# Kernel tuning notes

Hardware: AMD Instinct MI355X
Metric: run time of the kernel (lower is better)

Reference implementation:

```python
import jax, jax.numpy as jnp
import numpy as np

HIDDEN = 1024
SCALE = float(np.sqrt(HIDDEN))  # canonical sqrt(d) scale factor


def setup_inputs() -> dict:
    key = jax.random.key(0)
    ks = jax.random.split(key, 10)
    B, S, D = 4, 2048, HIDDEN
    bound = 1.0 / np.sqrt(D)  # torch Linear default init range
    inp = {
        "q": jax.random.normal(ks[0], (B, S, D), dtype=jnp.float32),
        "k": jax.random.normal(ks[1], (B, S, D), dtype=jnp.float32),
        "v": jax.random.normal(ks[2], (B, S, D), dtype=jnp.float32),
        "mask": jnp.zeros((B, S, S), dtype=bool),  # unused by original forward
        "Wq": jax.random.uniform(ks[3], (D, D), jnp.float32, -bound, bound),
        "bq": jax.random.uniform(ks[4], (D,), jnp.float32, -bound, bound),
        "Wk": jax.random.uniform(ks[5], (D, D), jnp.float32, -bound, bound),
        "bk": jax.random.uniform(ks[6], (D,), jnp.float32, -bound, bound),
        "Wv": jax.random.uniform(ks[7], (D, D), jnp.float32, -bound, bound),
        "bv": jax.random.uniform(ks[8], (D,), jnp.float32, -bound, bound),
    }
    return inp


def reference(q, k, v, mask, Wq, bq, Wk, bk, Wv, bv):
    # torch Linear: y = x @ W.T + b
    qp = jnp.einsum("bsd,ed->bse", q, Wq) + bq  # [B,S,D]
    kp = jnp.einsum("bsd,ed->bse", k, Wk) + bk
    vp = jnp.einsum("bsd,ed->bse", v, Wv) + bv
    scores = jnp.einsum("bqd,bkd->bqk", qp, kp) / SCALE  # [B,S,S]
    attn = jax.nn.softmax(scores, axis=-1)
    # dropout with p=0 (dropout_p undefined in source) -> identity
    out = jnp.einsum("bqk,bkd->bqd", attn, vp)  # [B,S,D]
    return out
```

## Files before the change

kernel.cpp:

```cpp
#include <hip/hip_runtime.h>

#define S_ 2048
#define D_ 1024
#define MTOT 8192

typedef __attribute__((ext_vector_type(8))) short bf16x8;
typedef __attribute__((ext_vector_type(8))) unsigned short ush8;
typedef __attribute__((ext_vector_type(4))) unsigned short ush4;
typedef __attribute__((ext_vector_type(4))) float f32x4;

__device__ __forceinline__ unsigned short f2bf(float x) {
    unsigned u = __builtin_bit_cast(unsigned, x);
    u += 0x7fffu + ((u >> 16) & 1u);
    return (unsigned short)(u >> 16);
}

__device__ __forceinline__ void async16(const unsigned short* g, unsigned short* l) {
    __builtin_amdgcn_global_load_lds(
        (const __attribute__((address_space(1))) unsigned int*)(g),
        (__attribute__((address_space(3))) unsigned int*)(l),
        16, 0, 0);
}

#define FENCE() asm volatile("" ::: "memory")
#define SBAR()  __builtin_amdgcn_s_barrier()
#define SCHED0() __builtin_amdgcn_sched_barrier(0)

template<int N> __device__ __forceinline__ void waitv();
template<> __device__ __forceinline__ void waitv<0>() { asm volatile("s_waitcnt vmcnt(0)" ::: "memory"); }
template<> __device__ __forceinline__ void waitv<2>() { asm volatile("s_waitcnt vmcnt(2)" ::: "memory"); }
template<> __device__ __forceinline__ void waitv<4>() { asm volatile("s_waitcnt vmcnt(4)" ::: "memory"); }

__device__ __forceinline__ int xcd_remap(int id, int nwg) {
    return (id & 7) * (nwg >> 3) + (id >> 3);
}

__global__ __launch_bounds__(256)
void tobf16_kernel(const float* __restrict__ s0, const float* __restrict__ s1,
                   const float* __restrict__ s2, const float* __restrict__ s3,
                   const float* __restrict__ s4, const float* __restrict__ s5,
                   unsigned short* __restrict__ d0, unsigned short* __restrict__ d1,
                   unsigned short* __restrict__ d2, unsigned short* __restrict__ d3,
                   unsigned short* __restrict__ d4, unsigned short* __restrict__ d5)
{
    const float* src; unsigned short* dst; size_t n;
    switch (blockIdx.y) {
        case 0: src = s0; dst = d0; n = (size_t)MTOT * D_; break;
        case 1: src = s1; dst = d1; n = (size_t)MTOT * D_; break;
        case 2: src = s2; dst = d2; n = (size_t)MTOT * D_; break;
        case 3: src = s3; dst = d3; n = (size_t)D_ * D_;   break;
        case 4: src = s4; dst = d4; n = (size_t)D_ * D_;   break;
        default: src = s5; dst = d5; n = (size_t)D_ * D_;  break;
    }
    size_t base = ((size_t)blockIdx.x * 256 + threadIdx.x) * 8;
    if (base >= n) return;
    float4 a = *reinterpret_cast<const float4*>(src + base);
    float4 b = *reinterpret_cast<const float4*>(src + base + 4);
    ush8 h;
    h[0] = f2bf(a.x); h[1] = f2bf(a.y); h[2] = f2bf(a.z); h[3] = f2bf(a.w);
    h[4] = f2bf(b.x); h[5] = f2bf(b.y); h[6] = f2bf(b.z); h[7] = f2bf(b.w);
    *reinterpret_cast<ush8*>(dst + base) = h;
}

template<int EPI, int BM>
__device__ __forceinline__ void gemm_body(
    unsigned short* As, unsigned short* Bs,
    const unsigned short* __restrict__ Ag, const unsigned short* __restrict__ Bg,
    const float* __restrict__ bias,
    float* __restrict__ Cf, unsigned short* __restrict__ Cbf,
    int K, float alpha, int ldc, int m0, int n0, size_t coff)
{
    constexpr int WM    = BM / 2;
    constexpr int MI    = WM / 16;
    constexpr int MIH   = MI / 2;
    constexpr int ASLAB = BM / 64;
    constexpr int ABUF  = BM * 64;
    constexpr int BBUF  = 256 * 64;

    const int t = threadIdx.x;
    const int w = t >> 6, lane = t & 63;
    const int wr = w >> 2, wc = w & 3;
    const int lr = lane & 15, lk4 = lane >> 4;

    const int crow = t >> 3;
    const int cj   = ((t & 7) ^ ((t >> 4) & 3)) * 8;

    auto stA = [&](int buf, int s, int kt) {
        async16(Ag + (size_t)(m0 + s * 64 + crow) * K + kt * 64 + cj,
                As + buf * ABUF + s * 4096 + w * 512);
    };
    auto stB = [&](int buf, int s, int kt) {
        async16(Bg + (size_t)(n0 + s * 64 + crow) * K + kt * 64 + cj,
                Bs + buf * BBUF + s * 4096 + w * 512);
    };
    auto rdA = [&](int buf, int rr, int kk) -> bf16x8 {
        const int phys = ((kk * 4 + lk4) ^ ((rr >> 1) & 3)) * 8;
        return *reinterpret_cast<const bf16x8*>(As + buf * ABUF + rr * 64 + phys);
    };
    auto rdB = [&](int buf, int rr, int kk) -> bf16x8 {
        const int phys = ((kk * 4 + lk4) ^ ((rr >> 1) & 3)) * 8;
        return *reinterpret_cast<const bf16x8*>(Bs + buf * BBUF + rr * 64 + phys);
    };

    f32x4 acc[MI][4];
    const f32x4 z4 = {0.f, 0.f, 0.f, 0.f};
#pragma unroll
    for (int i = 0; i < MI; i++)
#pragma unroll
        for (int j = 0; j < 4; j++) acc[i][j] = z4;

    const int NT = K >> 6;

#pragma unroll
    for (int s = 0; s < ASLAB; ++s) stA(0, s, 0);
#pragma unroll
    for (int s = 0; s < 4; ++s)     stB(0, s, 0);
#pragma unroll
    for (int s = 0; s < ASLAB; ++s) stA(1, s, 1);
    waitv<ASLAB>(); SCHED0(); SBAR(); FENCE();

    for (int kt = 0; kt < NT; ++kt) {
        const int cur = kt & 1;
        if (kt + 1 < NT) {
#pragma unroll
            for (int s = 0; s < 4; ++s) stB(cur ^ 1, s, kt + 1);
        }

        bf16x8 bfr[4][2];
#pragma unroll
        for (int ni = 0; ni < 4; ++ni)
#pragma unroll
            for (int kk = 0; kk < 2; ++kk)
                bfr[ni][kk] = rdB(cur, wc * 64 + ni * 16 + lr, kk);

        bf16x8 af[MIH][2];
#pragma unroll
        for (int mi = 0; mi < MIH; ++mi)
#pragma unroll
            for (int kk = 0; kk < 2; ++kk)
                af[mi][kk] = rdA(cur, wr * WM + mi * 16 + lr, kk);
        __builtin_amdgcn_s_setprio(1);
#pragma unroll
        for (int mi = 0; mi < MIH; ++mi)
#pragma unroll
            for (int ni = 0; ni < 4; ++ni)
#pragma unroll
                for (int kk = 0; kk < 2; ++kk)
                    acc[mi][ni] = __builtin_amdgcn_mfma_f32_16x16x32_bf16(af[mi][kk], bfr[ni][kk], acc[mi][ni], 0, 0, 0);
        __builtin_amdgcn_s_setprio(0);

#pragma unroll
        for (int mi = 0; mi < MIH; ++mi)
#pragma unroll
            for (int kk = 0; kk < 2; ++kk)
                af[mi][kk] = rdA(cur, wr * WM + (MIH + mi) * 16 + lr, kk);
        __builtin_amdgcn_s_setprio(1);
#pragma unroll
        for (int mi = 0; mi < MIH; ++mi)
#pragma unroll
            for (int ni = 0; ni < 4; ++ni)
#pragma unroll
                for (int kk = 0; kk < 2; ++kk)
                    acc[MIH + mi][ni] = __builtin_amdgcn_mfma_f32_16x16x32_bf16(af[mi][kk], bfr[ni][kk], acc[MIH + mi][ni], 0, 0, 0);
        __builtin_amdgcn_s_setprio(0);

        FENCE(); SBAR();
        if (kt + 2 < NT) {
#pragma unroll
            for (int s = 0; s < ASLAB; ++s) stA(cur, s, kt + 2);
            waitv<ASLAB>();
        } else if (kt + 1 < NT) {
            waitv<0>();
        }
        if (kt + 1 < NT) { SCHED0(); SBAR(); FENCE(); }
    }

#pragma unroll
    for (int mi = 0; mi < MI; ++mi) {
        const int mbase = m0 + wr * WM + mi * 16 + lk4 * 4;
#pragma unroll
        for (int ni = 0; ni < 4; ++ni) {
            const int nn = n0 + wc * 64 + ni * 16 + lr;
            if constexpr (EPI == 0) {
#pragma unroll
                for (int r = 0; r < 4; ++r)
                    Cf[coff + (size_t)(mbase + r) * ldc + nn] = alpha * acc[mi][ni][r];
            } else if constexpr (EPI == 1) {
                const float bb = bias[nn];
#pragma unroll
                for (int r = 0; r < 4; ++r)
                    Cbf[(size_t)(mbase + r) * ldc + nn] = f2bf(acc[mi][ni][r] + bb);
            } else {
                const float bb = bias[nn];
                const int batch = mbase >> 11, ss = mbase & 2047;
                ush4 hv;
#pragma unroll
                for (int r = 0; r < 4; ++r) hv[r] = f2bf(acc[mi][ni][r] + bb);
                *reinterpret_cast<ush4*>(Cbf + ((size_t)(batch << 10) + nn) * S_ + ss) = hv;
            }
        }
    }
}

__global__ __launch_bounds__(512, 2)
void proj256(const unsigned short* __restrict__ q, const unsigned short* __restrict__ k,
             const unsigned short* __restrict__ v,
             const unsigned short* __restrict__ wq, const unsigned short* __restrict__ wk,
             const unsigned short* __restrict__ wv,
             const float* __restrict__ bq, const float* __restrict__ bk,
             const float* __restrict__ bv,
             unsigned short* __restrict__ qp, unsigned short* __restrict__ kp,
             unsigned short* __restrict__ vT)
{
    __shared__ unsigned short As[2 * 256 * 64];
    __shared__ unsigned short Bs[2 * 256 * 64];
    int id = xcd_remap(blockIdx.x + 32 * (blockIdx.y + 4 * blockIdx.z), 32 * 4 * 3);
    const int bx = id % 32; id /= 32;
    const int by = id % 4;
    const int bz = id / 4;
    const unsigned short *A, *Bm; const float* bb; unsigned short* Ob;
    if (bz == 0)      { A = q; Bm = wq; bb = bq; Ob = qp; }
    else if (bz == 1) { A = k; Bm = wk; bb = bk; Ob = kp; }
    else              { A = v; Bm = wv; bb = bv; Ob = vT; }
    if (bz == 2)
        gemm_body<2, 256>(As, Bs, A, Bm, bb, nullptr, Ob, D_, 1.f, D_, bx * 256, by * 256, 0);
    else
        gemm_body<1, 256>(As, Bs, A, Bm, bb, nullptr, Ob, D_, 1.f, D_, bx * 256, by * 256, 0);
}

__global__ __launch_bounds__(512, 2)
void qk256(const unsigned short* __restrict__ qp, const unsigned short* __restrict__ kp,
           float* __restrict__ sc)
{
    __shared__ unsigned short As[2 * 256 * 64];
    __shared__ unsigned short Bs[2 * 256 * 64];
    int id = xcd_remap(blockIdx.x + 8 * (blockIdx.y + 8 * blockIdx.z), 8 * 8 * 4);
    const int bx = id % 8; id /= 8;
    const int by = id % 8;
    const int bz = id / 8;
    gemm_body<0, 256>(As, Bs, qp + (size_t)bz * S_ * D_, kp + (size_t)bz * S_ * D_,
                      nullptr, sc, nullptr, D_, 0.03125f, S_,
                      bx * 256, by * 256, (size_t)bz * S_ * S_);
}

__global__ __launch_bounds__(512, 2)
void pv128(const unsigned short* __restrict__ P, const unsigned short* __restrict__ vT,
           float* __restrict__ out)
{
    __shared__ unsigned short As[2 * 128 * 64];
    __shared__ unsigned short Bs[2 * 256 * 64];
    int id = xcd_remap(blockIdx.x + 16 * (blockIdx.y + 4 * blockIdx.z), 16 * 4 * 4);
    const int bx = id % 16; id /= 16;
    const int by = id % 4;
    const int bz = id / 4;
    gemm_body<0, 128>(As, Bs, P + (size_t)bz * S_ * S_, vT + (size_t)bz * D_ * S_,
                      nullptr, out, nullptr, S_, 1.f, D_,
                      bx * 128, by * 256, (size_t)bz * S_ * D_);
}

__global__ __launch_bounds__(256)
void softmax_kernel(const float* __restrict__ s, unsigned short* __restrict__ P)
{
    const size_t row = blockIdx.x;
    const int t = threadIdx.x;
    const float* sp = s + row * 2048 + (size_t)t * 8;
    float4 a = *reinterpret_cast<const float4*>(sp);
    float4 b = *reinterpret_cast<const float4*>(sp + 4);
    float x[8] = {a.x, a.y, a.z, a.w, b.x, b.y, b.z, b.w};

    float m = x[0];
    for (int j = 1; j < 8; j++) m = fmaxf(m, x[j]);
    for (int off = 1; off < 64; off <<= 1) m = fmaxf(m, __shfl_xor(m, off));
    __shared__ float redm[4], reds[4];
    const int w = t >> 6;
    if ((t & 63) == 0) redm[w] = m;
    __syncthreads();
    m = fmaxf(fmaxf(redm[0], redm[1]), fmaxf(redm[2], redm[3]));

    float e[8]; float sum = 0.f;
    for (int j = 0; j < 8; j++) { e[j] = __expf(x[j] - m); sum += e[j]; }
    for (int off = 1; off < 64; off <<= 1) sum += __shfl_xor(sum, off);
    if ((t & 63) == 0) reds[w] = sum;
    __syncthreads();
    sum = reds[0] + reds[1] + reds[2] + reds[3];
    const float inv = 1.0f / sum;

    ush8 h;
    for (int j = 0; j < 8; j++) h[j] = f2bf(e[j] * inv);
    *reinterpret_cast<ush8*>(P + row * 2048 + (size_t)t * 8) = h;
}

extern "C" void kernel_launch(void* const* d_in, const int* in_sizes, int n_in,
                              void* d_out, int out_size, void* d_ws, size_t ws_size,
                              hipStream_t stream)
{
    const float* q  = (const float*)d_in[0];
    const float* k  = (const float*)d_in[1];
    const float* v  = (const float*)d_in[2];
    const float* Wq = (const float*)d_in[4];
    const float* bq = (const float*)d_in[5];
    const float* Wk = (const float*)d_in[6];
    const float* bk = (const float*)d_in[7];
    const float* Wv = (const float*)d_in[8];
    const float* bv = (const float*)d_in[9];
    float* out = (float*)d_out;

    const size_t MB = (size_t)1 << 20;
    const size_t need = 198 * MB;
    if (ws_size < need) return;
    char* ws = (char*)d_ws;
    unsigned short* qbf  = (unsigned short*)(ws + 0 * MB);
    unsigned short* kbf  = (unsigned short*)(ws + 16 * MB);
    unsigned short* vbf  = (unsigned short*)(ws + 32 * MB);
    unsigned short* wqbf = (unsigned short*)(ws + 48 * MB);
    unsigned short* wkbf = (unsigned short*)(ws + 50 * MB);
    unsigned short* wvbf = (unsigned short*)(ws + 52 * MB);
    unsigned short* qp   = (unsigned short*)(ws + 54 * MB);
    unsigned short* kp   = (unsigned short*)(ws + 70 * MB);
    unsigned short* vT   = (unsigned short*)(ws + 86 * MB);
    float*          sc   = (float*)         (ws + 102 * MB);
    unsigned short* P    = (unsigned short*)(ws + 166 * MB);

    tobf16_kernel<<<dim3(4096, 6), dim3(256), 0, stream>>>(q, k, v, Wq, Wk, Wv,
                                                           qbf, kbf, vbf, wqbf, wkbf, wvbf);

    proj256<<<dim3(32, 4, 3), dim3(512), 0, stream>>>(qbf, kbf, vbf, wqbf, wkbf, wvbf,
                                                      bq, bk, bv, qp, kp, vT);

    qk256<<<dim3(8, 8, 4), dim3(512), 0, stream>>>(qp, kp, sc);

    softmax_kernel<<<dim3(MTOT), dim3(256), 0, stream>>>(sc, P);

    pv128<<<dim3(16, 4, 4), dim3(512), 0, stream>>>(P, vT, out);
}
```

Measured before the change: 233.2 us.

## Restructure GEMM pipeline with quarter-step prefetch, stacked weights, and interleaved QK output

The GEMM mainloop is split into four quarter-steps. Both A and B for tile kt+2 are prefetched, with the loads spread across those quarters, and the LDS swizzle gains an extra XOR bit to reduce bank conflicts. The projections now use stacked weights and biases with 128-row tiles in one 768-block launch. Q and K projections are written interleaved into one buffer, and qk reads it with a leading dimension of 2048. The goal is better overlap of loads with MFMA and better occupancy for the projection, at the cost of more barriers per k-step.

```diff
diff --git a/kernel.cpp b/kernel.cpp
--- a/kernel.cpp
+++ b/kernel.cpp
@@ -28,8 +28,8 @@
 
 template<int N> __device__ __forceinline__ void waitv();
 template<> __device__ __forceinline__ void waitv<0>() { asm volatile("s_waitcnt vmcnt(0)" ::: "memory"); }
-template<> __device__ __forceinline__ void waitv<2>() { asm volatile("s_waitcnt vmcnt(2)" ::: "memory"); }
-template<> __device__ __forceinline__ void waitv<4>() { asm volatile("s_waitcnt vmcnt(4)" ::: "memory"); }
+template<> __device__ __forceinline__ void waitv<6>() { asm volatile("s_waitcnt vmcnt(6)" ::: "memory"); }
+template<> __device__ __forceinline__ void waitv<8>() { asm volatile("s_waitcnt vmcnt(8)" ::: "memory"); }
 
 __device__ __forceinline__ int xcd_remap(int id, int nwg) {
     return (id & 7) * (nwg >> 3) + (id >> 3);
@@ -39,10 +39,24 @@
 void tobf16_kernel(const float* __restrict__ s0, const float* __restrict__ s1,
                    const float* __restrict__ s2, const float* __restrict__ s3,
                    const float* __restrict__ s4, const float* __restrict__ s5,
+                   const float* __restrict__ bq, const float* __restrict__ bk,
+                   const float* __restrict__ bv,
                    unsigned short* __restrict__ d0, unsigned short* __restrict__ d1,
                    unsigned short* __restrict__ d2, unsigned short* __restrict__ d3,
-                   unsigned short* __restrict__ d4, unsigned short* __restrict__ d5)
-{
+                   unsigned short* __restrict__ d4, unsigned short* __restrict__ d5,
+                   float* __restrict__ bias_out)
+{
+    if (blockIdx.y == 6) {
+        if (blockIdx.x != 0) return;
+        const int t = threadIdx.x;
+        for (int i = t; i < 768; i += 256) {
+            const int fidx = i * 4;
+            const float* src = (fidx < 1024) ? bq : (fidx < 2048) ? bk : bv;
+            reinterpret_cast<float4*>(bias_out)[i] =
+                reinterpret_cast<const float4*>(src)[(fidx & 1023) >> 2];
+        }
+        return;
+    }
     const float* src; unsigned short* dst; size_t n;
     switch (blockIdx.y) {
         case 0: src = s0; dst = d0; n = (size_t)MTOT * D_; break;
@@ -65,15 +79,17 @@
 template<int EPI, int BM>
 __device__ __forceinline__ void gemm_body(
     unsigned short* As, unsigned short* Bs,
-    const unsigned short* __restrict__ Ag, const unsigned short* __restrict__ Bg,
+    const unsigned short* __restrict__ Ag, int lda,
+    const unsigned short* __restrict__ Bg, int ldb,
     const float* __restrict__ bias,
     float* __restrict__ Cf, unsigned short* __restrict__ Cbf,
     int K, float alpha, int ldc, int m0, int n0, size_t coff)
 {
     constexpr int WM    = BM / 2;
     constexpr int MI    = WM / 16;
-    constexpr int MIH   = MI / 2;
+    constexpr int RQ    = MI / 4;
     constexpr int ASLAB = BM / 64;
+    constexpr int SC    = ASLAB + 4;
     constexpr int ABUF  = BM * 64;
     constexpr int BBUF  = 256 * 64;
 
@@ -83,22 +99,22 @@
     const int lr = lane & 15, lk4 = lane >> 4;
 
     const int crow = t >> 3;
-    const int cj   = ((t & 7) ^ ((t >> 4) & 3)) * 8;
+    const int cj = ((lane & 7) ^ ((lane >> 4) & 3) ^ (((lane >> 3) & 1) << 2)) * 8;
 
     auto stA = [&](int buf, int s, int kt) {
-        async16(Ag + (size_t)(m0 + s * 64 + crow) * K + kt * 64 + cj,
+        async16(Ag + (size_t)(m0 + s * 64 + crow) * lda + kt * 64 + cj,
                 As + buf * ABUF + s * 4096 + w * 512);
     };
     auto stB = [&](int buf, int s, int kt) {
-        async16(Bg + (size_t)(n0 + s * 64 + crow) * K + kt * 64 + cj,
+        async16(Bg + (size_t)(n0 + s * 64 + crow) * ldb + kt * 64 + cj,
                 Bs + buf * BBUF + s * 4096 + w * 512);
     };
     auto rdA = [&](int buf, int rr, int kk) -> bf16x8 {
-        const int phys = ((kk * 4 + lk4) ^ ((rr >> 1) & 3)) * 8;
+        const int phys = ((kk * 4 + lk4) ^ ((rr >> 1) & 3) ^ ((rr & 1) << 2)) * 8;
         return *reinterpret_cast<const bf16x8*>(As + buf * ABUF + rr * 64 + phys);
     };
     auto rdB = [&](int buf, int rr, int kk) -> bf16x8 {
-        const int phys = ((kk * 4 + lk4) ^ ((rr >> 1) & 3)) * 8;
+        const int phys = ((kk * 4 + lk4) ^ ((rr >> 1) & 3) ^ ((rr & 1) << 2)) * 8;
         return *reinterpret_cast<const bf16x8*>(Bs + buf * BBUF + rr * 64 + phys);
     };
 
@@ -117,62 +133,71 @@
     for (int s = 0; s < 4; ++s)     stB(0, s, 0);
 #pragma unroll
     for (int s = 0; s < ASLAB; ++s) stA(1, s, 1);
-    waitv<ASLAB>(); SCHED0(); SBAR(); FENCE();
+#pragma unroll
+    for (int s = 0; s < 4; ++s)     stB(1, s, 1);
+    waitv<SC>(); SCHED0(); SBAR(); FENCE();
 
     for (int kt = 0; kt < NT; ++kt) {
         const int cur = kt & 1;
-        if (kt + 1 < NT) {
-#pragma unroll
-            for (int s = 0; s < 4; ++s) stB(cur ^ 1, s, kt + 1);
-        }
+        const bool pf = (kt + 2 < NT);
 
         bf16x8 bfr[4][2];
+        bf16x8 af[RQ][2];
+
 #pragma unroll
         for (int ni = 0; ni < 4; ++ni)
 #pragma unroll
             for (int kk = 0; kk < 2; ++kk)
                 bfr[ni][kk] = rdB(cur, wc * 64 + ni * 16 + lr, kk);
-
-        bf16x8 af[MIH][2];
-#pragma unroll
-        for (int mi = 0; mi < MIH; ++mi)
+#pragma unroll
+        for (int rr = 0; rr < RQ; ++rr)
 #pragma unroll
             for (int kk = 0; kk < 2; ++kk)
-                af[mi][kk] = rdA(cur, wr * WM + mi * 16 + lr, kk);
+                af[rr][kk] = rdA(cur, wr * WM + rr * 16 + lr, kk);
+        FENCE(); SBAR();
         __builtin_amdgcn_s_setprio(1);
 #pragma unroll
-        for (int mi = 0; mi < MIH; ++mi)
+        for (int rr = 0; rr < RQ; ++rr)
 #pragma unroll
             for (int ni = 0; ni < 4; ++ni)
 #pragma unroll
                 for (int kk = 0; kk < 2; ++kk)
-                    acc[mi][ni] = __builtin_amdgcn_mfma_f32_16x16x32_bf16(af[mi][kk], bfr[ni][kk], acc[mi][ni], 0, 0, 0);
+                    acc[rr][ni] = __builtin_amdgcn_mfma_f32_16x16x32_bf16(af[rr][kk], bfr[ni][kk], acc[rr][ni], 0, 0, 0);
         __builtin_amdgcn_s_setprio(0);
-
-#pragma unroll
-        for (int mi = 0; mi < MIH; ++mi)
-#pragma unroll
-            for (int kk = 0; kk < 2; ++kk)
-                af[mi][kk] = rdA(cur, wr * WM + (MIH + mi) * 16 + lr, kk);
-        __builtin_amdgcn_s_setprio(1);
-#pragma unroll
-        for (int mi = 0; mi < MIH; ++mi)
-#pragma unroll
-            for (int ni = 0; ni < 4; ++ni)
+        FENCE(); SBAR();
+
+#pragma unroll
+        for (int q = 1; q < 4; ++q) {
+#pragma unroll
+            for (int rr = 0; rr < RQ; ++rr)
 #pragma unroll
                 for (int kk = 0; kk < 2; ++kk)
-                    acc[MIH + mi][ni] = __builtin_amdgcn_mfma_f32_16x16x32_bf16(af[mi][kk], bfr[ni][kk], acc[MIH + mi][ni], 0, 0, 0);
-        __builtin_amdgcn_s_setprio(0);
-
-        FENCE(); SBAR();
-        if (kt + 2 < NT) {
-#pragma unroll
-            for (int s = 0; s < ASLAB; ++s) stA(cur, s, kt + 2);
-            waitv<ASLAB>();
+                    af[rr][kk] = rdA(cur, wr * WM + (q * RQ + rr) * 16 + lr, kk);
+            if (pf) {
+                if (q == 1)      { stB(cur, 0, kt + 2); stB(cur, 1, kt + 2); }
+                else if (q == 2) { stB(cur, 2, kt + 2); stB(cur, 3, kt + 2); }
+                else if (BM == 256) { stA(cur, 0, kt + 2); stA(cur, 2, kt + 2); }
+            }
+            FENCE(); SBAR();
+            __builtin_amdgcn_s_setprio(1);
+#pragma unroll
+            for (int rr = 0; rr < RQ; ++rr)
+#pragma unroll
+                for (int ni = 0; ni < 4; ++ni)
+#pragma unroll
+                    for (int kk = 0; kk < 2; ++kk)
+                        acc[q * RQ + rr][ni] = __builtin_amdgcn_mfma_f32_16x16x32_bf16(af[rr][kk], bfr[ni][kk], acc[q * RQ + rr][ni], 0, 0, 0);
+            __builtin_amdgcn_s_setprio(0);
+            FENCE(); SBAR();
+        }
+
+        if (pf) {
+            if (BM == 256) { stA(cur, 1, kt + 2); stA(cur, 3, kt + 2); }
+            else           { stA(cur, 0, kt + 2); stA(cur, 1, kt + 2); }
+            waitv<SC>(); SCHED0(); SBAR(); FENCE();
         } else if (kt + 1 < NT) {
-            waitv<0>();
+            waitv<0>(); SCHED0(); SBAR(); FENCE();
         }
-        if (kt + 1 < NT) { SCHED0(); SBAR(); FENCE(); }
     }
 
 #pragma unroll
@@ -192,53 +217,48 @@
                     Cbf[(size_t)(mbase + r) * ldc + nn] = f2bf(acc[mi][ni][r] + bb);
             } else {
                 const float bb = bias[nn];
+                const int nn2 = nn - 2048;
                 const int batch = mbase >> 11, ss = mbase & 2047;
                 ush4 hv;
 #pragma unroll
                 for (int r = 0; r < 4; ++r) hv[r] = f2bf(acc[mi][ni][r] + bb);
-                *reinterpret_cast<ush4*>(Cbf + ((size_t)(batch << 10) + nn) * S_ + ss) = hv;
+                *reinterpret_cast<ush4*>(Cbf + ((size_t)(batch << 10) + nn2) * S_ + ss) = hv;
             }
         }
     }
 }
 
 __global__ __launch_bounds__(512, 2)
-void proj256(const unsigned short* __restrict__ q, const unsigned short* __restrict__ k,
-             const unsigned short* __restrict__ v,
-             const unsigned short* __restrict__ wq, const unsigned short* __restrict__ wk,
-             const unsigned short* __restrict__ wv,
-             const float* __restrict__ bq, const float* __restrict__ bk,
-             const float* __restrict__ bv,
-             unsigned short* __restrict__ qp, unsigned short* __restrict__ kp,
-             unsigned short* __restrict__ vT)
+void proj_fused(const unsigned short* __restrict__ qbf, const unsigned short* __restrict__ kbf,
+                const unsigned short* __restrict__ vbf, const unsigned short* __restrict__ wstk,
+                const float* __restrict__ bias, unsigned short* __restrict__ QP2,
+                unsigned short* __restrict__ vT)
+{
+    __shared__ unsigned short As[2 * 128 * 64];
+    __shared__ unsigned short Bs[2 * 256 * 64];
+    int id = xcd_remap(blockIdx.x + 64 * blockIdx.y, 768);
+    const int bx = id % 64;
+    const int by = id / 64;
+    const unsigned short* A = (by < 4) ? qbf : (by < 8) ? kbf : vbf;
+    if (by < 8)
+        gemm_body<1, 128>(As, Bs, A, D_, wstk, D_, bias, nullptr, QP2,
+                          D_, 1.f, 2048, bx * 128, by * 256, 0);
+    else
+        gemm_body<2, 128>(As, Bs, A, D_, wstk, D_, bias, nullptr, vT,
+                          D_, 1.f, 0, bx * 128, by * 256, 0);
+}
+
+__global__ __launch_bounds__(512, 2)
+void qk256(const unsigned short* __restrict__ QP2, float* __restrict__ sc)
 {
     __shared__ unsigned short As[2 * 256 * 64];
     __shared__ unsigned short Bs[2 * 256 * 64];
-    int id = xcd_remap(blockIdx.x + 32 * (blockIdx.y + 4 * blockIdx.z), 32 * 4 * 3);
-    const int bx = id % 32; id /= 32;
-    const int by = id % 4;
-    const int bz = id / 4;
-    const unsigned short *A, *Bm; const float* bb; unsigned short* Ob;
-    if (bz == 0)      { A = q; Bm = wq; bb = bq; Ob = qp; }
-    else if (bz == 1) { A = k; Bm = wk; bb = bk; Ob = kp; }
-    else              { A = v; Bm = wv; bb = bv; Ob = vT; }
-    if (bz == 2)
-        gemm_body<2, 256>(As, Bs, A, Bm, bb, nullptr, Ob, D_, 1.f, D_, bx * 256, by * 256, 0);
-    else
-        gemm_body<1, 256>(As, Bs, A, Bm, bb, nullptr, Ob, D_, 1.f, D_, bx * 256, by * 256, 0);
-}
-
-__global__ __launch_bounds__(512, 2)
-void qk256(const unsigned short* __restrict__ qp, const unsigned short* __restrict__ kp,
-           float* __restrict__ sc)
-{
-    __shared__ unsigned short As[2 * 256 * 64];
-    __shared__ unsigned short Bs[2 * 256 * 64];
-    int id = xcd_remap(blockIdx.x + 8 * (blockIdx.y + 8 * blockIdx.z), 8 * 8 * 4);
+    int id = xcd_remap(blockIdx.x + 8 * (blockIdx.y + 8 * blockIdx.z), 256);
     const int bx = id % 8; id /= 8;
     const int by = id % 8;
     const int bz = id / 8;
-    gemm_body<0, 256>(As, Bs, qp + (size_t)bz * S_ * D_, kp + (size_t)bz * S_ * D_,
+    const unsigned short* base = QP2 + (size_t)bz * S_ * 2048;
+    gemm_body<0, 256>(As, Bs, base, 2048, base + 1024, 2048,
                       nullptr, sc, nullptr, D_, 0.03125f, S_,
                       bx * 256, by * 256, (size_t)bz * S_ * S_);
 }
@@ -249,11 +269,12 @@
 {
     __shared__ unsigned short As[2 * 128 * 64];
     __shared__ unsigned short Bs[2 * 256 * 64];
-    int id = xcd_remap(blockIdx.x + 16 * (blockIdx.y + 4 * blockIdx.z), 16 * 4 * 4);
+    int id = xcd_remap(blockIdx.x + 16 * (blockIdx.y + 4 * blockIdx.z), 256);
     const int bx = id % 16; id /= 16;
     const int by = id % 4;
     const int bz = id / 4;
-    gemm_body<0, 128>(As, Bs, P + (size_t)bz * S_ * S_, vT + (size_t)bz * D_ * S_,
+    gemm_body<0, 128>(As, Bs, P + (size_t)bz * S_ * S_, S_,
+                      vT + (size_t)bz * D_ * S_, S_,
                       nullptr, out, nullptr, S_, 1.f, D_,
                       bx * 128, by * 256, (size_t)bz * S_ * D_);
 }
@@ -306,28 +327,25 @@
     float* out = (float*)d_out;
 
     const size_t MB = (size_t)1 << 20;
-    const size_t need = 198 * MB;
-    if (ws_size < need) return;
+    if (ws_size < 200 * MB) return;
     char* ws = (char*)d_ws;
     unsigned short* qbf  = (unsigned short*)(ws + 0 * MB);
     unsigned short* kbf  = (unsigned short*)(ws + 16 * MB);
     unsigned short* vbf  = (unsigned short*)(ws + 32 * MB);
-    unsigned short* wqbf = (unsigned short*)(ws + 48 * MB);
-    unsigned short* wkbf = (unsigned short*)(ws + 50 * MB);
-    unsigned short* wvbf = (unsigned short*)(ws + 52 * MB);
-    unsigned short* qp   = (unsigned short*)(ws + 54 * MB);
-    unsigned short* kp   = (unsigned short*)(ws + 70 * MB);
-    unsigned short* vT   = (unsigned short*)(ws + 86 * MB);
-    float*          sc   = (float*)         (ws + 102 * MB);
-    unsigned short* P    = (unsigned short*)(ws + 166 * MB);
-
-    tobf16_kernel<<<dim3(4096, 6), dim3(256), 0, stream>>>(q, k, v, Wq, Wk, Wv,
-                                                           qbf, kbf, vbf, wqbf, wkbf, wvbf);
-
-    proj256<<<dim3(32, 4, 3), dim3(512), 0, stream>>>(qbf, kbf, vbf, wqbf, wkbf, wvbf,
-                                                      bq, bk, bv, qp, kp, vT);
-
-    qk256<<<dim3(8, 8, 4), dim3(512), 0, stream>>>(qp, kp, sc);
+    unsigned short* wstk = (unsigned short*)(ws + 48 * MB);
+    float*          bst  = (float*)         (ws + 54 * MB);
+    unsigned short* QP2  = (unsigned short*)(ws + 56 * MB);
+    unsigned short* vT   = (unsigned short*)(ws + 88 * MB);
+    float*          sc   = (float*)         (ws + 104 * MB);
+    unsigned short* P    = (unsigned short*)(ws + 168 * MB);
+
+    tobf16_kernel<<<dim3(4096, 7), dim3(256), 0, stream>>>(
+        q, k, v, Wq, Wk, Wv, bq, bk, bv,
+        qbf, kbf, vbf, wstk, wstk + (size_t)D_ * D_, wstk + 2 * (size_t)D_ * D_, bst);
+
+    proj_fused<<<dim3(64, 12), dim3(512), 0, stream>>>(qbf, kbf, vbf, wstk, bst, QP2, vT);
+
+    qk256<<<dim3(8, 8, 4), dim3(512), 0, stream>>>(QP2, sc);
 
     softmax_kernel<<<dim3(MTOT), dim3(256), 0, stream>>>(sc, P);
 
```

Measured after the change: 221.3 us. -5.1%, faster.
